# Kernel tuning notes

Hardware: AMD Instinct MI355X
Metric: run time of the kernel (lower is better)

Reference implementation:

```python
import jax, jax.numpy as jnp
import numpy as np

DIM = 1024
D_STATE = 16

def setup_inputs() -> dict:
    key = jax.random.key(0)
    kx, ka, kd = jax.random.split(key, 3)
    x = jax.random.normal(kx, (4, 8192, DIM), dtype=jnp.float32)
    A = jax.random.normal(ka, (DIM, D_STATE), dtype=jnp.float32)
    D = jax.random.normal(kd, (D_STATE, DIM), dtype=jnp.float32)
    return {"x": x, "A": A, "D": D}

def reference(x, A, D):
    # x: [B, N, C]; A: [C, S]; D: [S, C]
    x_state = jnp.einsum('bnc,cs->bns', x, A)        # [B, N, S]
    x_state = jnp.cumsum(x_state, axis=1)            # prefix sum over sequence
    out = jnp.einsum('bns,sc->bnc', x_state, D)      # [B, N, C]
    return out
```

## Files before the change

kernel.cpp:

```cpp
#include <hip/hip_runtime.h>

#define DIM   1024
#define DST   16
#define NSEQ  8192
#define NB    4

#define K1_MT   64
#define K1_KC   128
#define K1_KCP  132

__global__ __launch_bounds__(256) void k1_gemm(const float* __restrict__ x,
                                               const float* __restrict__ A,
                                               float* __restrict__ T) {
    __shared__ float xs[K1_MT * K1_KCP];
    __shared__ float at[DST * K1_KCP];
    const int t  = threadIdx.x;
    const int b  = blockIdx.x >> 7;
    const int n0 = (blockIdx.x & 127) * K1_MT;
    const int s  = t & 15;
    const int mg = t >> 4;

    const float* xrow = x + ((long)(b * NSEQ + n0)) * DIM;

    float acc0 = 0.f, acc1 = 0.f, acc2 = 0.f, acc3 = 0.f;

    for (int kc = 0; kc < DIM; kc += K1_KC) {
        {
            const int q  = t & 31;
            const int r0 = t >> 5;
            #pragma unroll
            for (int it = 0; it < 8; ++it) {
                const int m = it * 8 + r0;
                const float4 v = *(const float4*)(xrow + (long)m * DIM + kc + 4 * q);
                *(float4*)&xs[m * K1_KCP + 4 * q] = v;
            }
        }
        {
            #pragma unroll
            for (int it = 0; it < 8; ++it) {
                const int idx = it * 256 + t;
                const int kl  = idx >> 4;
                const int ss  = idx & 15;
                at[ss * K1_KCP + kl] = A[(kc + kl) * DST + ss];
            }
        }
        __syncthreads();

        #pragma unroll 4
        for (int kq = 0; kq < K1_KC / 4; ++kq) {
            const float4 a  = *(const float4*)&at[s * K1_KCP + 4 * kq];
            const float4 x0 = *(const float4*)&xs[(mg * 4 + 0) * K1_KCP + 4 * kq];
            const float4 x1 = *(const float4*)&xs[(mg * 4 + 1) * K1_KCP + 4 * kq];
            const float4 x2 = *(const float4*)&xs[(mg * 4 + 2) * K1_KCP + 4 * kq];
            const float4 x3 = *(const float4*)&xs[(mg * 4 + 3) * K1_KCP + 4 * kq];
            acc0 += x0.x * a.x + x0.y * a.y + x0.z * a.z + x0.w * a.w;
            acc1 += x1.x * a.x + x1.y * a.y + x1.z * a.z + x1.w * a.w;
            acc2 += x2.x * a.x + x2.y * a.y + x2.z * a.z + x2.w * a.w;
            acc3 += x3.x * a.x + x3.y * a.y + x3.z * a.z + x3.w * a.w;
        }
        __syncthreads();
    }

    const float4 o = make_float4(acc0, acc1, acc2, acc3);
    *(float4*)&T[((long)(b * DST + s)) * NSEQ + n0 + mg * 4] = o;
}

__global__ __launch_bounds__(256) void k2_scan(float* __restrict__ T) {
    __shared__ float sums[256];
    const int t = threadIdx.x;
    const int b = blockIdx.x >> 4;
    const int s = blockIdx.x & 15;
    float* row = T + ((long)(b * DST + s)) * NSEQ;
    const int base = t * 32;

    float v[32];
    #pragma unroll
    for (int j = 0; j < 8; ++j) {
        const float4 f = *(const float4*)&row[base + 4 * j];
        v[4 * j + 0] = f.x; v[4 * j + 1] = f.y;
        v[4 * j + 2] = f.z; v[4 * j + 3] = f.w;
    }
    float run = 0.f;
    #pragma unroll
    for (int i = 0; i < 32; ++i) { run += v[i]; v[i] = run; }

    sums[t] = run;
    const float total = run;
    __syncthreads();
    for (int off = 1; off < 256; off <<= 1) {
        const float u = (t >= off) ? sums[t - off] : 0.f;
        __syncthreads();
        sums[t] += u;
        __syncthreads();
    }
    const float excl = sums[t] - total;

    #pragma unroll
    for (int j = 0; j < 8; ++j) {
        const float4 f = make_float4(v[4 * j + 0] + excl, v[4 * j + 1] + excl,
                                     v[4 * j + 2] + excl, v[4 * j + 3] + excl);
        *(float4*)&row[base + 4 * j] = f;
    }
}

#define K3_W 64

__global__ __launch_bounds__(256) void k3_out(const float* __restrict__ T,
                                              const float* __restrict__ D,
                                              float* __restrict__ out) {
    __shared__ float sp[K3_W * 20];
    const int t  = threadIdx.x;
    const int b  = blockIdx.x >> 7;
    const int n0 = (blockIdx.x & 127) * K3_W;

    #pragma unroll
    for (int j = 0; j < 4; ++j) {
        const int idx = j * 256 + t;
        const int ss  = idx >> 6;
        const int nn  = idx & 63;
        sp[nn * 20 + ss] = T[((long)(b * DST + ss)) * NSEQ + n0 + nn];
    }

    float4 dreg[16];
    #pragma unroll
    for (int ss = 0; ss < 16; ++ss)
        dreg[ss] = *(const float4*)&D[ss * DIM + 4 * t];

    __syncthreads();

    float* ob = out + ((long)(b * NSEQ + n0)) * DIM + 4 * t;
    for (int r = 0; r < K3_W; ++r) {
        const float4 s0 = *(const float4*)&sp[r * 20 + 0];
        const float4 s1 = *(const float4*)&sp[r * 20 + 4];
        const float4 s2 = *(const float4*)&sp[r * 20 + 8];
        const float4 s3 = *(const float4*)&sp[r * 20 + 12];
        const float sv[16] = {s0.x, s0.y, s0.z, s0.w, s1.x, s1.y, s1.z, s1.w,
                              s2.x, s2.y, s2.z, s2.w, s3.x, s3.y, s3.z, s3.w};
        float4 o = make_float4(0.f, 0.f, 0.f, 0.f);
        #pragma unroll
        for (int ss = 0; ss < 16; ++ss) {
            o.x += sv[ss] * dreg[ss].x;
            o.y += sv[ss] * dreg[ss].y;
            o.z += sv[ss] * dreg[ss].z;
            o.w += sv[ss] * dreg[ss].w;
        }
        *(float4*)(ob + (long)r * DIM) = o;
    }
}

extern "C" void kernel_launch(void* const* d_in, const int* in_sizes, int n_in,
                              void* d_out, int out_size, void* d_ws, size_t ws_size,
                              hipStream_t stream) {
    const float* x = (const float*)d_in[0];
    const float* A = (const float*)d_in[1];
    const float* D = (const float*)d_in[2];
    float* out = (float*)d_out;
    float* T   = (float*)d_ws;

    k1_gemm<<<dim3(NB * 128), dim3(256), 0, stream>>>(x, A, T);
    k2_scan<<<dim3(NB * DST), dim3(256), 0, stream>>>(T);
    k3_out <<<dim3(NB * 128), dim3(256), 0, stream>>>(T, D, out);
}
```

Baseline: 274.0 us.

## Use split-bf16 MFMA for x·A projection and wave-shuffle scan

```diff
diff --git a/kernel.cpp b/kernel.cpp
--- a/kernel.cpp
+++ b/kernel.cpp
@@ -5,68 +5,82 @@
 #define NSEQ  8192
 #define NB    4
 
-#define K1_MT   64
-#define K1_KC   128
-#define K1_KCP  132
+typedef __attribute__((ext_vector_type(8))) short  short8;
+typedef __attribute__((ext_vector_type(4))) float  floatx4;
 
-__global__ __launch_bounds__(256) void k1_gemm(const float* __restrict__ x,
+__device__ inline unsigned bf16_rne_bits(float f) {
+    unsigned u = __float_as_uint(f);
+    return (u + 0x7fffu + ((u >> 16) & 1u)) >> 16;
+}
+
+#define KP 1032
+
+__global__ __launch_bounds__(256) void k1_mfma(const float* __restrict__ x,
                                                const float* __restrict__ A,
                                                float* __restrict__ T) {
-    __shared__ float xs[K1_MT * K1_KCP];
-    __shared__ float at[DST * K1_KCP];
+    __shared__ unsigned short abHi[DST * KP];
+    __shared__ unsigned short abLo[DST * KP];
     const int t  = threadIdx.x;
     const int b  = blockIdx.x >> 7;
-    const int n0 = (blockIdx.x & 127) * K1_MT;
-    const int s  = t & 15;
-    const int mg = t >> 4;
+    const int n0 = (blockIdx.x & 127) * 64;
 
-    const float* xrow = x + ((long)(b * NSEQ + n0)) * DIM;
+    for (int i = t; i < DIM * DST; i += 256) {
+        const int s = i & 15, k = i >> 4;
+        const float a = A[i];
+        const unsigned hb = bf16_rne_bits(a);
+        const float ah = __uint_as_float(hb << 16);
+        const unsigned lb = bf16_rne_bits(a - ah);
+        abHi[s * KP + k] = (unsigned short)hb;
+        abLo[s * KP + k] = (unsigned short)lb;
+    }
+    __syncthreads();
 
-    float acc0 = 0.f, acc1 = 0.f, acc2 = 0.f, acc3 = 0.f;
+    const int wave = t >> 6;
+    const int lane = t & 63;
+    const int m    = lane & 15;
+    const int q    = lane >> 4;
 
-    for (int kc = 0; kc < DIM; kc += K1_KC) {
-        {
-            const int q  = t & 31;
-            const int r0 = t >> 5;
-            #pragma unroll
-            for (int it = 0; it < 8; ++it) {
-                const int m = it * 8 + r0;
-                const float4 v = *(const float4*)(xrow + (long)m * DIM + kc + 4 * q);
-                *(float4*)&xs[m * K1_KCP + 4 * q] = v;
-            }
+    const int row = n0 + wave * 16 + m;
+    const float* xp = x + ((long)(b * NSEQ + row)) * DIM + q * 8;
+    const unsigned short* bh = &abHi[m * KP + q * 8];
+    const unsigned short* bl = &abLo[m * KP + q * 8];
+
+    floatx4 acc = {0.f, 0.f, 0.f, 0.f};
+
+    float4 c0 = *(const float4*)(xp);
+    float4 c1 = *(const float4*)(xp + 4);
+
+    for (int step = 0; step < 32; ++step) {
+        const int ns = (step + 1) & 31;
+        const float4 p0 = *(const float4*)(xp + ns * 32);
+        const float4 p1 = *(const float4*)(xp + ns * 32 + 4);
+
+        short8 ahi, alo;
+        const float cf[8] = {c0.x, c0.y, c0.z, c0.w, c1.x, c1.y, c1.z, c1.w};
+        #pragma unroll
+        for (int j = 0; j < 8; ++j) {
+            const unsigned hb = bf16_rne_bits(cf[j]);
+            const float fh = __uint_as_float(hb << 16);
+            const unsigned lb = bf16_rne_bits(cf[j] - fh);
+            ahi[j] = (short)hb;
+            alo[j] = (short)lb;
         }
-        {
-            #pragma unroll
-            for (int it = 0; it < 8; ++it) {
-                const int idx = it * 256 + t;
-                const int kl  = idx >> 4;
-                const int ss  = idx & 15;
-                at[ss * K1_KCP + kl] = A[(kc + kl) * DST + ss];
-            }
-        }
-        __syncthreads();
+        const short8 bhi = *(const short8*)(bh + step * 32);
+        const short8 blo = *(const short8*)(bl + step * 32);
 
-        #pragma unroll 4
-        for (int kq = 0; kq < K1_KC / 4; ++kq) {
-            const float4 a  = *(const float4*)&at[s * K1_KCP + 4 * kq];
-            const float4 x0 = *(const float4*)&xs[(mg * 4 + 0) * K1_KCP + 4 * kq];
-            const float4 x1 = *(const float4*)&xs[(mg * 4 + 1) * K1_KCP + 4 * kq];
-            const float4 x2 = *(const float4*)&xs[(mg * 4 + 2) * K1_KCP + 4 * kq];
-            const float4 x3 = *(const float4*)&xs[(mg * 4 + 3) * K1_KCP + 4 * kq];
-            acc0 += x0.x * a.x + x0.y * a.y + x0.z * a.z + x0.w * a.w;
-            acc1 += x1.x * a.x + x1.y * a.y + x1.z * a.z + x1.w * a.w;
-            acc2 += x2.x * a.x + x2.y * a.y + x2.z * a.z + x2.w * a.w;
-            acc3 += x3.x * a.x + x3.y * a.y + x3.z * a.z + x3.w * a.w;
-        }
-        __syncthreads();
+        acc = __builtin_amdgcn_mfma_f32_16x16x32_bf16(ahi, bhi, acc, 0, 0, 0);
+        acc = __builtin_amdgcn_mfma_f32_16x16x32_bf16(alo, bhi, acc, 0, 0, 0);
+        acc = __builtin_amdgcn_mfma_f32_16x16x32_bf16(ahi, blo, acc, 0, 0, 0);
+
+        c0 = p0; c1 = p1;
     }
 
-    const float4 o = make_float4(acc0, acc1, acc2, acc3);
-    *(float4*)&T[((long)(b * DST + s)) * NSEQ + n0 + mg * 4] = o;
+    float* tp = &T[((long)(b * DST + m)) * NSEQ + n0 + wave * 16 + q * 4];
+    *(floatx4*)tp = acc;
 }
 
 __global__ __launch_bounds__(256) void k2_scan(float* __restrict__ T) {
-    __shared__ float sums[256];
+    __shared__ float wsum[4];
     const int t = threadIdx.x;
     const int b = blockIdx.x >> 4;
     const int s = blockIdx.x & 15;
@@ -84,16 +98,21 @@
     #pragma unroll
     for (int i = 0; i < 32; ++i) { run += v[i]; v[i] = run; }
 
-    sums[t] = run;
-    const float total = run;
+    const int lane = t & 63;
+    float sc = run;
+    #pragma unroll
+    for (int off = 1; off < 64; off <<= 1) {
+        const float u = __shfl_up(sc, off, 64);
+        if (lane >= off) sc += u;
+    }
+    const int w = t >> 6;
+    if (lane == 63) wsum[w] = sc;
     __syncthreads();
-    for (int off = 1; off < 256; off <<= 1) {
-        const float u = (t >= off) ? sums[t - off] : 0.f;
-        __syncthreads();
-        sums[t] += u;
-        __syncthreads();
-    }
-    const float excl = sums[t] - total;
+
+    float woff = 0.f;
+    #pragma unroll
+    for (int i = 0; i < 4; ++i) woff += (i < w) ? wsum[i] : 0.f;
+    const float excl = woff + sc - run;
 
     #pragma unroll
     for (int j = 0; j < 8; ++j) {
@@ -157,7 +176,7 @@
     float* out = (float*)d_out;
     float* T   = (float*)d_ws;
 
-    k1_gemm<<<dim3(NB * 128), dim3(256), 0, stream>>>(x, A, T);
+    k1_mfma<<<dim3(NB * 128), dim3(256), 0, stream>>>(x, A, T);
     k2_scan<<<dim3(NB * DST), dim3(256), 0, stream>>>(T);
     k3_out <<<dim3(NB * 128), dim3(256), 0, stream>>>(T, D, out);
 }
```

Result: slower. 288.7 us (+5.4%).
